# Kernel optimization log

Hardware: AMD Instinct MI355X
Metric: run time of the kernel (lower is better)

The kernel has to match this reference:

```python
import jax, jax.numpy as jnp
import numpy as np

BATCH = 2048
BUCKETS = 100000
DIM = 64

def setup_inputs() -> dict:
    key = jax.random.key(0)
    k1, k2 = jax.random.split(key)
    inputs = jax.random.uniform(k1, (BATCH, BUCKETS), dtype=jnp.float32)
    embeddings = jax.random.normal(k2, (BUCKETS, DIM), dtype=jnp.float32)
    return {"inputs": inputs, "embeddings": embeddings}

def reference(inputs, embeddings):
    # K.dot(inputs, embeddings): [B, buckets] @ [buckets, dim] -> [B, dim]
    out = jnp.matmul(inputs, embeddings)
    # mean=True branch: divide by count of active buckets, zero where empty
    s = jnp.sum(inputs, axis=-1, keepdims=True)  # [B, 1]
    out = jnp.where(s > 0, out / s, jnp.zeros_like(out))
    return out
```

## Files before the change

### kernel.cpp

```cpp
#include <hip/hip_runtime.h>
#include <hip/hip_bf16.h>

#define BATCH 2048
#define KDIM  100000
#define DIM   64
#define NKB   (KDIM / 32)
#define KP    64
#define RPB   128
#define NRB   (BATCH / RPB)

typedef __attribute__((ext_vector_type(8))) short  short8;
typedef __attribute__((ext_vector_type(4))) float  f32x4;

__device__ __forceinline__ unsigned short f2bf(float f) {
    union { float f; unsigned int u; } v; v.f = f;
    unsigned int u = v.u;
    u += 0x7FFFu + ((u >> 16) & 1u);
    return (unsigned short)(u >> 16);
}

__global__ __launch_bounds__(256)
void hashemb_pack(const float* __restrict__ emb, unsigned short* __restrict__ pB) {
    const int kb   = blockIdx.x;
    const int t    = threadIdx.x >> 6;
    const int lane = threadIdx.x & 63;
    const int col  = t * 16 + (lane & 15);
    const int krow = kb * 32 + (lane >> 4) * 8;

    short8 w;
    #pragma unroll
    for (int j = 0; j < 8; ++j)
        w[j] = (short)f2bf(emb[(size_t)(krow + j) * DIM + col]);

    *(short8*)&pB[(((size_t)kb * 4 + t) * 64 + lane) * 8] = w;
}

__global__ __launch_bounds__(256, 4)
void hashemb_matmul(const float* __restrict__ inp,
                    const unsigned short* __restrict__ pB,
                    float* __restrict__ part,
                    float* __restrict__ rsp) {
    const int tid  = threadIdx.x;
    const int lane = tid & 63;
    const int wid  = tid >> 6;

    const int wg  = blockIdx.x;
    const int xcd = wg & 7;
    const int pos = wg >> 3;
    const int kp  = xcd * (KP / 8) + (pos >> 4);
    const int rb  = pos & 15;

    const int base = NKB / KP;
    const int rem  = NKB % KP;
    const int cnt  = base + (kp < rem ? 1 : 0);
    const int kb0  = kp * base + (kp < rem ? kp : rem);

    const int rowbase = rb * RPB + wid * 32;
    const int r0   = rowbase + (lane & 15);
    const int kgrp = lane >> 4;

    const float* ap0 = inp + (size_t)r0 * KDIM + (size_t)kb0 * 32 + kgrp * 8;
    const float* ap1 = ap0 + (size_t)16 * KDIM;
    const unsigned short* bp = pB + ((size_t)kb0 * 4 * 64 + lane) * 8;

    f32x4 acc0[4], acc1[4];
    #pragma unroll
    for (int t = 0; t < 4; ++t) { acc0[t] = (f32x4)0.0f; acc1[t] = (f32x4)0.0f; }
    float lsum0 = 0.0f, lsum1 = 0.0f;

    auto loadA = [&](int c, f32x4& xa, f32x4& xb, f32x4& ya, f32x4& yb) {
        const int cc = (c < cnt) ? c : cnt - 1;
        xa = *(const f32x4*)(ap0 + (size_t)cc * 32);
        xb = *(const f32x4*)(ap0 + (size_t)cc * 32 + 4);
        ya = *(const f32x4*)(ap1 + (size_t)cc * 32);
        yb = *(const f32x4*)(ap1 + (size_t)cc * 32 + 4);
    };

    auto step = [&](int c, f32x4& xa, f32x4& xb, f32x4& ya, f32x4& yb) {
        if (c < cnt) {
            short8 af0, af1;
            #pragma unroll
            for (int j = 0; j < 4; ++j) {
                af0[j] = (short)f2bf(xa[j]);  af0[4 + j] = (short)f2bf(xb[j]);
                af1[j] = (short)f2bf(ya[j]);  af1[4 + j] = (short)f2bf(yb[j]);
            }
            lsum0 += xa[0] + xa[1] + xa[2] + xa[3] + xb[0] + xb[1] + xb[2] + xb[3];
            lsum1 += ya[0] + ya[1] + ya[2] + ya[3] + yb[0] + yb[1] + yb[2] + yb[3];
            loadA(c + 2, xa, xb, ya, yb);
            const unsigned short* b = bp + (size_t)c * 2048;
            #pragma unroll
            for (int t = 0; t < 4; ++t) {
                const short8 bf = *(const short8*)(b + t * 512);
                acc0[t] = __builtin_amdgcn_mfma_f32_16x16x32_bf16(af0, bf, acc0[t], 0, 0, 0);
                acc1[t] = __builtin_amdgcn_mfma_f32_16x16x32_bf16(af1, bf, acc1[t], 0, 0, 0);
            }
        }
    };

    f32x4 x0a, x0b, y0a, y0b;
    f32x4 x1a, x1b, y1a, y1b;
    loadA(0, x0a, x0b, y0a, y0b);
    loadA(1, x1a, x1b, y1a, y1b);

    for (int c = 0; c < cnt; c += 2) {
        step(c,     x0a, x0b, y0a, y0b);
        step(c + 1, x1a, x1b, y1a, y1b);
    }

    lsum0 += __shfl_xor(lsum0, 16, 64);
    lsum0 += __shfl_xor(lsum0, 32, 64);
    lsum1 += __shfl_xor(lsum1, 16, 64);
    lsum1 += __shfl_xor(lsum1, 32, 64);
    if (lane < 16) {
        rsp[(size_t)kp * BATCH + rowbase + lane]      = lsum0;
        rsp[(size_t)kp * BATCH + rowbase + 16 + lane] = lsum1;
    }

    float* po = part + (size_t)kp * BATCH * DIM;
    #pragma unroll
    for (int t = 0; t < 4; ++t) {
        const int col = t * 16 + (lane & 15);
        #pragma unroll
        for (int j = 0; j < 4; ++j) {
            const int row = rowbase + kgrp * 4 + j;
            po[(size_t)row * DIM + col]        = acc0[t][j];
            po[(size_t)(row + 16) * DIM + col] = acc1[t][j];
        }
    }
}

__global__ __launch_bounds__(256)
void hashemb_rsreduce(const float* __restrict__ rsp, float* __restrict__ rs) {
    const int row = blockIdx.x * 256 + threadIdx.x;
    float s = 0.0f;
    #pragma unroll 8
    for (int p = 0; p < KP; ++p) s += rsp[(size_t)p * BATCH + row];
    rs[row] = s;
}

__global__ __launch_bounds__(256)
void hashemb_finalize(const float* __restrict__ part, const float* __restrict__ rs,
                      float* __restrict__ out) {
    const int i4 = blockIdx.x * 256 + threadIdx.x;
    const float s = rs[i4 >> 4];
    f32x4 o = (f32x4)0.0f;
    #pragma unroll 8
    for (int p = 0; p < KP; ++p)
        o += *(const f32x4*)(part + (size_t)p * BATCH * DIM + (size_t)i4 * 4);
    const float inv = (s > 0.0f) ? (1.0f / s) : 0.0f;
    o *= inv;
    *(f32x4*)(out + (size_t)i4 * 4) = o;
}

extern "C" void kernel_launch(void* const* d_in, const int* in_sizes, int n_in,
                              void* d_out, int out_size, void* d_ws, size_t ws_size,
                              hipStream_t stream) {
    const float* inp = (const float*)d_in[0];
    const float* emb = (const float*)d_in[1];
    float* out = (float*)d_out;

    float* rs  = (float*)d_ws;
    float* rsp = (float*)((char*)d_ws + 8192);
    float* part = (float*)((char*)d_ws + 532480);
    unsigned short* pB = (unsigned short*)((char*)d_ws + 34086912);

    hashemb_pack<<<NKB, 256, 0, stream>>>(emb, pB);

    hashemb_matmul<<<NRB * KP, 256, 0, stream>>>(inp, pB, part, rsp);

    hashemb_rsreduce<<<BATCH / 256, 256, 0, stream>>>(rsp, rs);

    hashemb_finalize<<<(BATCH * DIM / 4) / 256, 256, 0, stream>>>(part, rs, out);
}
```

Baseline: 216.9 us.

## Stream A tiles into LDS with async global_load_lds double buffering, fewer K-splits

```diff
diff --git a/kernel.cpp b/kernel.cpp
--- a/kernel.cpp
+++ b/kernel.cpp
@@ -5,9 +5,10 @@
 #define KDIM  100000
 #define DIM   64
 #define NKB   (KDIM / 32)
-#define KP    64
-#define RPB   128
-#define NRB   (BATCH / RPB)
+#define KP    16
+#define NRB   32
+#define SS    4
+#define NSS   49
 
 typedef __attribute__((ext_vector_type(8))) short  short8;
 typedef __attribute__((ext_vector_type(4))) float  f32x4;
@@ -17,6 +18,12 @@
     unsigned int u = v.u;
     u += 0x7FFFu + ((u >> 16) & 1u);
     return (unsigned short)(u >> 16);
+}
+
+__device__ __forceinline__ void glds16(const float* src, unsigned char* lds) {
+    __builtin_amdgcn_global_load_lds(
+        (const __attribute__((address_space(1))) void*)src,
+        (__attribute__((address_space(3))) void*)lds, 16, 0, 0);
 }
 
 __global__ __launch_bounds__(256)
@@ -35,11 +42,13 @@
     *(short8*)&pB[(((size_t)kb * 4 + t) * 64 + lane) * 8] = w;
 }
 
-__global__ __launch_bounds__(256, 4)
+__global__ __launch_bounds__(256, 2)
 void hashemb_matmul(const float* __restrict__ inp,
                     const unsigned short* __restrict__ pB,
                     float* __restrict__ part,
                     float* __restrict__ rsp) {
+    __shared__ __align__(1024) unsigned char smem[4][2][8192];
+
     const int tid  = threadIdx.x;
     const int lane = tid & 63;
     const int wid  = tid >> 6;
@@ -47,84 +56,108 @@
     const int wg  = blockIdx.x;
     const int xcd = wg & 7;
     const int pos = wg >> 3;
-    const int kp  = xcd * (KP / 8) + (pos >> 4);
-    const int rb  = pos & 15;
-
-    const int base = NKB / KP;
-    const int rem  = NKB % KP;
-    const int cnt  = base + (kp < rem ? 1 : 0);
-    const int kb0  = kp * base + (kp < rem ? kp : rem);
-
-    const int rowbase = rb * RPB + wid * 32;
-    const int r0   = rowbase + (lane & 15);
-    const int kgrp = lane >> 4;
-
-    const float* ap0 = inp + (size_t)r0 * KDIM + (size_t)kb0 * 32 + kgrp * 8;
-    const float* ap1 = ap0 + (size_t)16 * KDIM;
-    const unsigned short* bp = pB + ((size_t)kb0 * 4 * 64 + lane) * 8;
-
-    f32x4 acc0[4], acc1[4];
-    #pragma unroll
-    for (int t = 0; t < 4; ++t) { acc0[t] = (f32x4)0.0f; acc1[t] = (f32x4)0.0f; }
-    float lsum0 = 0.0f, lsum1 = 0.0f;
-
-    auto loadA = [&](int c, f32x4& xa, f32x4& xb, f32x4& ya, f32x4& yb) {
-        const int cc = (c < cnt) ? c : cnt - 1;
-        xa = *(const f32x4*)(ap0 + (size_t)cc * 32);
-        xb = *(const f32x4*)(ap0 + (size_t)cc * 32 + 4);
-        ya = *(const f32x4*)(ap1 + (size_t)cc * 32);
-        yb = *(const f32x4*)(ap1 + (size_t)cc * 32 + 4);
+    const int kp  = xcd * 2 + (pos >> 5);
+    const int rb  = pos & 31;
+
+    const int cbase = NKB / KP;
+    const int rem   = NKB % KP;
+    const int cnt   = cbase + (kp < rem ? 1 : 0);
+    const int kb0   = kp * cbase + (kp < rem ? kp : rem);
+    const int kbEnd = kb0 + cnt;
+
+    const int rowbase = rb * 64 + wid * 16;
+
+    const int rsub = lane >> 5;
+    const int gcol = lane & 31;
+    const int frow = lane & 15;
+    const int g    = lane >> 4;
+    const int sw   = lane & 7;
+
+    const float* srcrow[8];
+    #pragma unroll
+    for (int i = 0; i < 8; ++i) {
+        const int r = 2 * i + rsub;
+        srcrow[i] = inp + (size_t)(rowbase + r) * KDIM + ((gcol ^ (r & 7)) << 2);
+    }
+
+    unsigned char* cur = &smem[wid][0][0];
+    unsigned char* nxt = &smem[wid][1][0];
+
+    auto ssStart = [&](int s) {
+        int b = kb0 + s * SS;
+        return (b > NKB - SS) ? (NKB - SS) : b;
     };
-
-    auto step = [&](int c, f32x4& xa, f32x4& xb, f32x4& ya, f32x4& yb) {
-        if (c < cnt) {
-            short8 af0, af1;
+    auto issue = [&](int base, unsigned char* buf) {
+        #pragma unroll
+        for (int i = 0; i < 8; ++i)
+            glds16(srcrow[i] + (size_t)base * 32, buf + i * 1024);
+    };
+
+    f32x4 acc[4];
+    #pragma unroll
+    for (int t = 0; t < 4; ++t) acc[t] = (f32x4)0.0f;
+    float lsum = 0.0f;
+
+    issue(kb0, cur);
+
+    for (int s = 0; s < NSS; ++s) {
+        const int base = ssStart(s);
+        const int lo   = kb0 + s * SS;
+
+        short8 Br[4][4];
+        #pragma unroll
+        for (int q = 0; q < SS; ++q) {
+            const unsigned short* bq = pB + (size_t)(base + q) * 2048 + (size_t)lane * 8;
             #pragma unroll
-            for (int j = 0; j < 4; ++j) {
-                af0[j] = (short)f2bf(xa[j]);  af0[4 + j] = (short)f2bf(xb[j]);
-                af1[j] = (short)f2bf(ya[j]);  af1[4 + j] = (short)f2bf(yb[j]);
+            for (int t = 0; t < 4; ++t)
+                Br[q][t] = *(const short8*)(bq + t * 512);
+        }
+        __builtin_amdgcn_sched_barrier(0);
+
+        if (s + 1 < NSS) {
+            issue(ssStart(s + 1), nxt);
+            asm volatile("s_waitcnt vmcnt(8)" ::: "memory");
+        } else {
+            asm volatile("s_waitcnt vmcnt(0)" ::: "memory");
+        }
+        __builtin_amdgcn_sched_barrier(0);
+
+        #pragma unroll
+        for (int q = 0; q < SS; ++q) {
+            const int c = base + q;
+            if (c >= lo && c < kbEnd) {
+                const int jb = (q << 3) + (g << 1);
+                const f32x4 xa = *(const f32x4*)(cur + frow * 512 + (((jb    ) ^ sw) << 4));
+                const f32x4 xb = *(const f32x4*)(cur + frow * 512 + (((jb + 1) ^ sw) << 4));
+                short8 af;
+                #pragma unroll
+                for (int j = 0; j < 4; ++j) {
+                    af[j]     = (short)f2bf(xa[j]);
+                    af[4 + j] = (short)f2bf(xb[j]);
+                }
+                lsum += xa[0] + xa[1] + xa[2] + xa[3]
+                      + xb[0] + xb[1] + xb[2] + xb[3];
+                #pragma unroll
+                for (int t = 0; t < 4; ++t)
+                    acc[t] = __builtin_amdgcn_mfma_f32_16x16x32_bf16(af, Br[q][t], acc[t], 0, 0, 0);
             }
-            lsum0 += xa[0] + xa[1] + xa[2] + xa[3] + xb[0] + xb[1] + xb[2] + xb[3];
-            lsum1 += ya[0] + ya[1] + ya[2] + ya[3] + yb[0] + yb[1] + yb[2] + yb[3];
-            loadA(c + 2, xa, xb, ya, yb);
-            const unsigned short* b = bp + (size_t)c * 2048;
-            #pragma unroll
-            for (int t = 0; t < 4; ++t) {
-                const short8 bf = *(const short8*)(b + t * 512);
-                acc0[t] = __builtin_amdgcn_mfma_f32_16x16x32_bf16(af0, bf, acc0[t], 0, 0, 0);
-                acc1[t] = __builtin_amdgcn_mfma_f32_16x16x32_bf16(af1, bf, acc1[t], 0, 0, 0);
-            }
-        }
-    };
-
-    f32x4 x0a, x0b, y0a, y0b;
-    f32x4 x1a, x1b, y1a, y1b;
-    loadA(0, x0a, x0b, y0a, y0b);
-    loadA(1, x1a, x1b, y1a, y1b);
-
-    for (int c = 0; c < cnt; c += 2) {
-        step(c,     x0a, x0b, y0a, y0b);
-        step(c + 1, x1a, x1b, y1a, y1b);
+        }
+
+        unsigned char* tmp = cur; cur = nxt; nxt = tmp;
     }
 
-    lsum0 += __shfl_xor(lsum0, 16, 64);
-    lsum0 += __shfl_xor(lsum0, 32, 64);
-    lsum1 += __shfl_xor(lsum1, 16, 64);
-    lsum1 += __shfl_xor(lsum1, 32, 64);
-    if (lane < 16) {
-        rsp[(size_t)kp * BATCH + rowbase + lane]      = lsum0;
-        rsp[(size_t)kp * BATCH + rowbase + 16 + lane] = lsum1;
-    }
+    lsum += __shfl_xor(lsum, 16, 64);
+    lsum += __shfl_xor(lsum, 32, 64);
+    if (lane < 16) rsp[(size_t)kp * BATCH + rowbase + lane] = lsum;
 
     float* po = part + (size_t)kp * BATCH * DIM;
     #pragma unroll
     for (int t = 0; t < 4; ++t) {
-        const int col = t * 16 + (lane & 15);
+        const int col = t * 16 + frow;
         #pragma unroll
         for (int j = 0; j < 4; ++j) {
-            const int row = rowbase + kgrp * 4 + j;
-            po[(size_t)row * DIM + col]        = acc0[t][j];
-            po[(size_t)(row + 16) * DIM + col] = acc1[t][j];
+            const int row = rowbase + g * 4 + j;
+            po[(size_t)row * DIM + col] = acc[t][j];
         }
     }
 }
@@ -133,7 +166,7 @@
 void hashemb_rsreduce(const float* __restrict__ rsp, float* __restrict__ rs) {
     const int row = blockIdx.x * 256 + threadIdx.x;
     float s = 0.0f;
-    #pragma unroll 8
+    #pragma unroll
     for (int p = 0; p < KP; ++p) s += rsp[(size_t)p * BATCH + row];
     rs[row] = s;
 }
@@ -144,7 +177,7 @@
     const int i4 = blockIdx.x * 256 + threadIdx.x;
     const float s = rs[i4 >> 4];
     f32x4 o = (f32x4)0.0f;
-    #pragma unroll 8
+    #pragma unroll
     for (int p = 0; p < KP; ++p)
         o += *(const f32x4*)(part + (size_t)p * BATCH * DIM + (size_t)i4 * 4);
     const float inv = (s > 0.0f) ? (1.0f / s) : 0.0f;
@@ -159,10 +192,10 @@
     const float* emb = (const float*)d_in[1];
     float* out = (float*)d_out;
 
-    float* rs  = (float*)d_ws;
-    float* rsp = (float*)((char*)d_ws + 8192);
-    float* part = (float*)((char*)d_ws + 532480);
-    unsigned short* pB = (unsigned short*)((char*)d_ws + 34086912);
+    float* rs   = (float*)d_ws;
+    float* rsp  = (float*)((char*)d_ws + 8192);
+    float* part = (float*)((char*)d_ws + 139264);
+    unsigned short* pB = (unsigned short*)((char*)d_ws + 8527872);
 
     hashemb_pack<<<NKB, 256, 0, stream>>>(emb, pB);
 
```

After: 212.7 us. About the same (-1.9%).
